# Kernel tuning notes

Measured on AMD Instinct MI355X. Metric: run time of the kernel, lower is better.

## Reference

```python
import jax, jax.numpy as jnp
import numpy as np

NEG_SLOPE = 0.2  # PyG GATConv leaky_relu slope


def _embed(feats, W1, b1, W2, b2, Wc, bc):
    # collapse_esm (two plain Linears, no activation) then linear_comb
    esm = feats[..., 24:] @ W1 + b1
    esm = esm @ W2 + b2
    x = jnp.concatenate([feats[..., :24], esm], axis=-1)
    return x @ Wc + bc


def _gat_conv(x, src, dst, n, W, a_src, a_dst, b, concat):
    # PyG GATConv: project, per-edge attention logits, softmax over incoming edges at dst,
    # weighted scatter-sum. Self loops already included in (src, dst).
    H, C = a_src.shape
    h = (x @ W).reshape(-1, H, C)                 # [N,H,C]
    s = (h * a_src).sum(-1)                       # [N,H]
    d = (h * a_dst).sum(-1)                       # [N,H]
    e = jax.nn.leaky_relu(s[src] + d[dst], NEG_SLOPE)  # [E,H]
    m = jax.ops.segment_max(e, dst, num_segments=n)
    e = jnp.exp(e - m[dst])
    z = jax.ops.segment_sum(e, dst, num_segments=n)
    alpha = e / z[dst]                            # [E,H]
    out = jax.ops.segment_sum(h[src] * alpha[:, :, None], dst, num_segments=n)  # [N,H,C]
    out = out.reshape(n, H * C) if concat else out.mean(axis=1)
    return out + b


def setup_inputs() -> dict:
    key = jax.random.key(0)
    ks = jax.random.split(key, 24)
    N, E, B, F = 100000, 3200000, 8, 50
    NF, M1, M2, M3, CH = 1304, 652, 326, 350, 32
    L, H, HID = 3, 8, 4
    f32 = jnp.float32
    inp = {
        "node_features": jax.random.normal(ks[0], (N, NF), f32),
        "edge_index": jax.random.randint(ks[1], (2, E), 0, N, dtype=jnp.int32),
        "edge_attr": jax.random.normal(ks[2], (E, 8), f32),
        "frag_emb": jax.random.normal(ks[3], (B, F, NF), f32),
        "W_esm1": jax.random.normal(ks[4], (NF - 24, M1), f32) / np.sqrt(NF - 24),
        "b_esm1": jnp.zeros((M1,), f32),
        "W_esm2": jax.random.normal(ks[5], (M1, M2), f32) / np.sqrt(M1),
        "b_esm2": jnp.zeros((M2,), f32),
        "W_comb": jax.random.normal(ks[6], (M3, CH), f32) / np.sqrt(M3),
        "b_comb": jnp.zeros((CH,), f32),
        "gat1_W": jax.random.normal(ks[7], (L, CH, H * HID), f32) / np.sqrt(CH),
        "gat1_asrc": jax.random.normal(ks[8], (L, H, HID), f32) * 0.1,
        "gat1_adst": jax.random.normal(ks[9], (L, H, HID), f32) * 0.1,
        "gat1_b": jnp.zeros((L, H * HID), f32),
        "gat2_W": jax.random.normal(ks[10], (L, H * HID, CH), f32) / np.sqrt(H * HID),
        "gat2_asrc": jax.random.normal(ks[11], (L, 1, CH), f32) * 0.1,
        "gat2_adst": jax.random.normal(ks[12], (L, 1, CH), f32) * 0.1,
        "gat2_b": jnp.zeros((L, CH), f32),
        "W_fin": jax.random.normal(ks[13], (CH, 1), f32) / np.sqrt(CH),
        "b_fin": jnp.zeros((1,), f32),
    }
    return inp


def reference(node_features, edge_index, edge_attr, frag_emb,
              W_esm1, b_esm1, W_esm2, b_esm2, W_comb, b_comb,
              gat1_W, gat1_asrc, gat1_adst, gat1_b,
              gat2_W, gat2_asrc, gat2_adst, gat2_b,
              W_fin, b_fin):
    N = node_features.shape[0]
    loop = jnp.arange(N, dtype=edge_index.dtype)
    src = jnp.concatenate([edge_index[0], loop])  # self loops (PyG default)
    dst = jnp.concatenate([edge_index[1], loop])

    x = _embed(node_features, W_esm1, b_esm1, W_esm2, b_esm2, W_comb, b_comb)  # [N,32]
    for i in range(gat1_W.shape[0]):
        x = _gat_conv(x, src, dst, N, gat1_W[i], gat1_asrc[i], gat1_adst[i], gat1_b[i], True)
        x = jax.nn.elu(x)
        x = _gat_conv(x, src, dst, N, gat2_W[i], gat2_asrc[i], gat2_adst[i], gat2_b[i], False)

    ys = _embed(frag_emb, W_esm1, b_esm1, W_esm2, b_esm2, W_comb, b_comb)  # [B,F,32]
    B, F, C = ys.shape
    xb = x.reshape(B, N // B, C)                      # equal-size graphs
    A = jax.nn.softmax(jnp.einsum('bnd,bfd->bnf', xb, ys), axis=-1)
    p = jnp.einsum('bnf,bfd->bnd', A, ys)             # [B,n,32]
    return jax.nn.sigmoid(p @ W_fin + b_fin).squeeze(-1)  # [B,n]
```

## Files before the change

### kernel.cpp

```cpp
#include <hip/hip_runtime.h>
#include <hip/hip_bf16.h>

#define NF 1304
#define M1 652
#define M2 326
#define CH 32
#define NHEAD1 8
#define HID1 4
#define NLAYER 3
#define FRAG 50
#define NBATCH 8
#define DPAD 32

static inline int ceil_div(int a, int b){ return (a + b - 1)/b; }

__device__ __forceinline__ unsigned short f2h(float f){
  _Float16 h = (_Float16)f;
  unsigned short u;
  __builtin_memcpy(&u, &h, 2);
  return u;
}
__device__ __forceinline__ float h2f(unsigned short u){
  _Float16 h;
  __builtin_memcpy(&h, &u, 2);
  return (float)h;
}

#define TM 64
#define TN 64
#define TKK 16
__global__ __launch_bounds__(256) void gemm_bias(
    const float* __restrict__ A, int lda,
    const float* __restrict__ B, int ldb,
    const float* __restrict__ bias,
    float* __restrict__ C, int ldc,
    int M, int N, int K, int acc)
{
  __shared__ float As[TKK][TM + 1];
  __shared__ float Bs[TKK][TN];
  int tid = threadIdx.x;
  int tx = tid & 15, ty = tid >> 4;
  int row0 = blockIdx.y * TM, col0 = blockIdx.x * TN;
  float c[4][4] = {};
  for (int k0 = 0; k0 < K; k0 += TKK) {
    #pragma unroll
    for (int p = 0; p < 4; ++p) {
      int r = (tid >> 4) + p * 16;
      int kk = tid & 15;
      int gr = row0 + r, gk = k0 + kk;
      float v = 0.f;
      if (gr < M && gk < K) v = A[(long long)gr * lda + gk];
      As[kk][r] = v;
    }
    #pragma unroll
    for (int p = 0; p < 4; ++p) {
      int kk = (tid >> 6) + p * 4;
      int cc = tid & 63;
      int gk = k0 + kk, gc = col0 + cc;
      float v = 0.f;
      if (gk < K && gc < N) v = B[(long long)gk * ldb + gc];
      Bs[kk][cc] = v;
    }
    __syncthreads();
    #pragma unroll
    for (int kk = 0; kk < TKK; ++kk) {
      float a[4], b[4];
      #pragma unroll
      for (int i = 0; i < 4; ++i) a[i] = As[kk][ty + 16 * i];
      #pragma unroll
      for (int j = 0; j < 4; ++j) b[j] = Bs[kk][tx + 16 * j];
      #pragma unroll
      for (int i = 0; i < 4; ++i)
        #pragma unroll
        for (int j = 0; j < 4; ++j)
          c[i][j] += a[i] * b[j];
    }
    __syncthreads();
  }
  #pragma unroll
  for (int i = 0; i < 4; ++i) {
    int gr = row0 + ty + 16 * i;
    if (gr >= M) continue;
    #pragma unroll
    for (int j = 0; j < 4; ++j) {
      int gc = col0 + tx + 16 * j;
      if (gc >= N) continue;
      float v = c[i][j];
      if (bias) v += bias[gc];
      if (acc) v += C[(long long)gr * ldc + gc];
      C[(long long)gr * ldc + gc] = v;
    }
  }
}

__global__ void fold_misc_kernel(const float* __restrict__ Wc, const float* __restrict__ T1,
                                 const float* __restrict__ b1, const float* __restrict__ b2,
                                 const float* __restrict__ bc,
                                 float* __restrict__ Wbig, float* __restrict__ bfold)
{
  int tid = threadIdx.x;
  for (int i = tid; i < 24 * CH; i += 256) Wbig[i] = Wc[i];
  if (tid < CH) {
    float v = bc[tid];
    for (int k = 0; k < M2; ++k) v += b2[k] * Wc[(24 + k) * CH + tid];
    for (int i = 0; i < M1; ++i) v += b1[i] * T1[i * CH + tid];
    bfold[tid] = v;
  }
}

#define EK 64
__global__ __launch_bounds__(256) void gemm_n32(
    const float* __restrict__ A, int M, int K,
    const float* __restrict__ W, const float* __restrict__ bias,
    float* __restrict__ C)
{
  __shared__ float As[64][65];
  __shared__ float Ws[EK][32];
  int tid = threadIdx.x;
  int row0 = blockIdx.x * 64;
  int tx = tid & 7, ty = tid >> 3;
  float c0[4] = {}, c1[4] = {};
  for (int k0 = 0; k0 < K; k0 += EK) {
    #pragma unroll
    for (int p = 0; p < 4; ++p) {
      int q = tid + p * 256;
      int r = q >> 4, c4 = (q & 15) * 4;
      int gr = row0 + r, gk = k0 + c4;
      float4 v = make_float4(0.f, 0.f, 0.f, 0.f);
      if (gr < M) {
        if (gk + 3 < K) v = *(const float4*)&A[(long long)gr * K + gk];
        else {
          float t[4] = {0.f, 0.f, 0.f, 0.f};
          for (int i = 0; i < 4; ++i) if (gk + i < K) t[i] = A[(long long)gr * K + gk + i];
          v = make_float4(t[0], t[1], t[2], t[3]);
        }
      }
      As[r][c4 + 0] = v.x; As[r][c4 + 1] = v.y; As[r][c4 + 2] = v.z; As[r][c4 + 3] = v.w;
    }
    #pragma unroll
    for (int p = 0; p < 2; ++p) {
      int q = tid + p * 256;
      int r = q >> 3, c4 = (q & 7) * 4;
      int gk = k0 + r;
      float4 v = make_float4(0.f, 0.f, 0.f, 0.f);
      if (gk < K) v = *(const float4*)&W[(long long)gk * 32 + c4];
      *(float4*)&Ws[r][c4] = v;
    }
    __syncthreads();
    #pragma unroll
    for (int kk = 0; kk < EK; ++kk) {
      float4 b = *(const float4*)&Ws[kk][tx * 4];
      float a0 = As[ty * 2][kk], a1 = As[ty * 2 + 1][kk];
      c0[0] += a0 * b.x; c0[1] += a0 * b.y; c0[2] += a0 * b.z; c0[3] += a0 * b.w;
      c1[0] += a1 * b.x; c1[1] += a1 * b.y; c1[2] += a1 * b.z; c1[3] += a1 * b.w;
    }
    __syncthreads();
  }
  float4 bb = *(const float4*)&bias[tx * 4];
  int gr0 = row0 + ty * 2;
  if (gr0 < M) {
    float4 v = make_float4(c0[0] + bb.x, c0[1] + bb.y, c0[2] + bb.z, c0[3] + bb.w);
    *(float4*)&C[(long long)gr0 * 32 + tx * 4] = v;
  }
  if (gr0 + 1 < M) {
    float4 v = make_float4(c1[0] + bb.x, c1[1] + bb.y, c1[2] + bb.z, c1[3] + bb.w);
    *(float4*)&C[(long long)(gr0 + 1) * 32 + tx * 4] = v;
  }
}

__global__ void zero_deg_kernel(int* __restrict__ degp, long long n)
{
  long long i = (long long)blockIdx.x * 256 + threadIdx.x;
  if (i < n) degp[i] = 0;
}
__global__ void rank_kernel(const int* __restrict__ ei, int E,
                            int* __restrict__ degp, int* __restrict__ rank)
{
  int e = blockIdx.x * 256 + threadIdx.x;
  if (e < E) rank[e] = atomicAdd(&degp[(long long)ei[E + e] * DPAD], 1);
}
__global__ void partial_kernel(const int* __restrict__ degp, int N, int* __restrict__ partial)
{
  __shared__ int sd[256];
  int i = blockIdx.x * 256 + threadIdx.x;
  sd[threadIdx.x] = (i < N) ? degp[(long long)i * DPAD] : 0;
  __syncthreads();
  for (int off = 128; off > 0; off >>= 1) {
    if (threadIdx.x < off) sd[threadIdx.x] += sd[threadIdx.x + off];
    __syncthreads();
  }
  if (threadIdx.x == 0) partial[blockIdx.x] = sd[0];
}
__global__ void scanp_kernel(int* __restrict__ partial, int NB)
{
  __shared__ int sd[512];
  int t = threadIdx.x;
  int v = (t < NB) ? partial[t] : 0;
  sd[t] = v;
  __syncthreads();
  for (int off = 1; off < 512; off <<= 1) {
    int u = (t >= off) ? sd[t - off] : 0;
    __syncthreads();
    sd[t] += u;
    __syncthreads();
  }
  if (t < NB) partial[t] = sd[t] - v;
}
__global__ void scan_final_kernel(const int* __restrict__ degp, int N,
                                  const int* __restrict__ partial,
                                  int* __restrict__ rowptr)
{
  __shared__ int sd[256];
  int i = blockIdx.x * 256 + threadIdx.x;
  int t = threadIdx.x;
  int v = (i < N) ? degp[(long long)i * DPAD] : 0;
  sd[t] = v;
  __syncthreads();
  for (int off = 1; off < 256; off <<= 1) {
    int u = (t >= off) ? sd[t - off] : 0;
    __syncthreads();
    sd[t] += u;
    __syncthreads();
  }
  if (i < N) {
    int excl = partial[blockIdx.x] + sd[t] - v;
    rowptr[i] = excl;
    if (i == N - 1) rowptr[N] = excl + v;
  }
}
__global__ void scatter_plain_kernel(const int* __restrict__ ei, int E,
                                     const int* __restrict__ rowptr,
                                     const int* __restrict__ rank,
                                     int* __restrict__ csr)
{
  int e = blockIdx.x * 256 + threadIdx.x;
  if (e >= E) return;
  int dn = ei[E + e];
  csr[rowptr[dn] + rank[e]] = ei[e];
}

template<int H, int C>
__global__ __launch_bounds__(256) void proj_sd_kernel(
    const float* __restrict__ x, const float* __restrict__ W,
    const float* __restrict__ asrc, const float* __restrict__ adst,
    unsigned* __restrict__ hp, float* __restrict__ sv, float* __restrict__ dv, int N)
{
  __shared__ float Ws[CH][CH];
  __shared__ float al[2][CH];
  int tid = threadIdx.x;
  for (int i = tid; i < CH * CH; i += 256) Ws[i >> 5][i & 31] = W[i];
  if (tid < CH) { al[0][tid] = asrc[tid]; al[1][tid] = adst[tid]; }
  __syncthreads();
  int n = blockIdx.x * 256 + tid;
  if (n >= N) return;
  float xr[CH];
  #pragma unroll
  for (int j = 0; j < CH / 4; ++j) {
    float4 v = *(const float4*)&x[(long long)n * CH + j * 4];
    xr[j * 4] = v.x; xr[j * 4 + 1] = v.y; xr[j * 4 + 2] = v.z; xr[j * 4 + 3] = v.w;
  }
  float hr[CH] = {};
  #pragma unroll
  for (int c = 0; c < CH; ++c) {
    float xc = xr[c];
    #pragma unroll
    for (int j4 = 0; j4 < CH / 4; ++j4) {
      float4 w = *(const float4*)&Ws[c][j4 * 4];
      hr[j4 * 4] += xc * w.x; hr[j4 * 4 + 1] += xc * w.y;
      hr[j4 * 4 + 2] += xc * w.z; hr[j4 * 4 + 3] += xc * w.w;
    }
  }
  unsigned pk[16];
  #pragma unroll
  for (int j = 0; j < 16; ++j)
    pk[j] = (unsigned)f2h(hr[2 * j]) | ((unsigned)f2h(hr[2 * j + 1]) << 16);
  uint4* hq = (uint4*)&hp[(long long)n * 16];
  #pragma unroll
  for (int j = 0; j < 4; ++j)
    hq[j] = make_uint4(pk[4 * j], pk[4 * j + 1], pk[4 * j + 2], pk[4 * j + 3]);
  #pragma unroll
  for (int hh = 0; hh < H; ++hh) {
    float ss = 0.f, dd = 0.f;
    #pragma unroll
    for (int c = 0; c < C; ++c) {
      float v = hr[hh * C + c];
      ss += v * al[0][hh * C + c];
      dd += v * al[1][hh * C + c];
    }
    sv[(long long)n * H + hh] = ss;
    dv[(long long)n * H + hh] = dd;
  }
}

template<int H, int C>
__global__ __launch_bounds__(256) void gat_gather_kernel(
    const int* __restrict__ rowptr, const int* __restrict__ csr,
    const unsigned* __restrict__ hp, const float* __restrict__ sv,
    const float* __restrict__ dv, const float* __restrict__ bias,
    float* __restrict__ xout, int N, int do_elu)
{
  int wid = threadIdx.x >> 6;
  int lane = threadIdx.x & 63;
  int n = blockIdx.x * 4 + wid;
  if (n >= N) return;
  int cpair = lane & 15;
  int slot = lane >> 4;
  int hh = (C == HID1) ? (cpair >> 1) : 0;
  float dn = dv[(long long)n * H + hh];
  float acc0 = 0.f, acc1 = 0.f, z = 0.f;
  if (slot == 0) {
    float lg = sv[(long long)n * H + hh] + dn;
    lg = lg > 0.f ? lg : 0.2f * lg;
    float w = expf(lg);
    z = w;
    unsigned u = hp[(long long)n * 16 + cpair];
    acc0 = w * h2f((unsigned short)(u & 0xffff));
    acc1 = w * h2f((unsigned short)(u >> 16));
  }
  int start = rowptr[n], end = rowptr[n + 1];
  for (int base = start; base < end; base += 64) {
    int m = end - base; if (m > 64) m = 64;
    int idx = (base + lane < end) ? csr[base + lane] : 0;
    int k = slot;
    for (; k + 12 < m; k += 16) {
      int si0 = __shfl(idx, k, 64);
      int si1 = __shfl(idx, k + 4, 64);
      int si2 = __shfl(idx, k + 8, 64);
      int si3 = __shfl(idx, k + 12, 64);
      float s0 = sv[(long long)si0 * H + hh];
      float s1 = sv[(long long)si1 * H + hh];
      float s2 = sv[(long long)si2 * H + hh];
      float s3 = sv[(long long)si3 * H + hh];
      unsigned u0 = hp[(long long)si0 * 16 + cpair];
      unsigned u1 = hp[(long long)si1 * 16 + cpair];
      unsigned u2 = hp[(long long)si2 * 16 + cpair];
      unsigned u3 = hp[(long long)si3 * 16 + cpair];
      float lg0 = s0 + dn; lg0 = lg0 > 0.f ? lg0 : 0.2f * lg0;
      float lg1 = s1 + dn; lg1 = lg1 > 0.f ? lg1 : 0.2f * lg1;
      float lg2 = s2 + dn; lg2 = lg2 > 0.f ? lg2 : 0.2f * lg2;
      float lg3 = s3 + dn; lg3 = lg3 > 0.f ? lg3 : 0.2f * lg3;
      float w0 = expf(lg0), w1 = expf(lg1), w2 = expf(lg2), w3 = expf(lg3);
      z += (w0 + w1) + (w2 + w3);
      acc0 += w0 * h2f((unsigned short)(u0 & 0xffff))
            + w1 * h2f((unsigned short)(u1 & 0xffff))
            + w2 * h2f((unsigned short)(u2 & 0xffff))
            + w3 * h2f((unsigned short)(u3 & 0xffff));
      acc1 += w0 * h2f((unsigned short)(u0 >> 16))
            + w1 * h2f((unsigned short)(u1 >> 16))
            + w2 * h2f((unsigned short)(u2 >> 16))
            + w3 * h2f((unsigned short)(u3 >> 16));
    }
    for (; k < m; k += 4) {
      int si0 = __shfl(idx, k, 64);
      float s0 = sv[(long long)si0 * H + hh];
      unsigned u0 = hp[(long long)si0 * 16 + cpair];
      float lg0 = s0 + dn; lg0 = lg0 > 0.f ? lg0 : 0.2f * lg0;
      float w0 = expf(lg0);
      z += w0;
      acc0 += w0 * h2f((unsigned short)(u0 & 0xffff));
      acc1 += w0 * h2f((unsigned short)(u0 >> 16));
    }
  }
  acc0 += __shfl_xor(acc0, 16, 64); acc0 += __shfl_xor(acc0, 32, 64);
  acc1 += __shfl_xor(acc1, 16, 64); acc1 += __shfl_xor(acc1, 32, 64);
  z    += __shfl_xor(z, 16, 64);    z    += __shfl_xor(z, 32, 64);
  if (slot == 0) {
    int ch = cpair * 2;
    float v0 = acc0 / z + bias[ch];
    float v1 = acc1 / z + bias[ch + 1];
    if (do_elu) {
      v0 = v0 > 0.f ? v0 : (expf(v0) - 1.f);
      v1 = v1 > 0.f ? v1 : (expf(v1) - 1.f);
    }
    *(float2*)&xout[(long long)n * 32 + ch] = make_float2(v0, v1);
  }
}

__global__ __launch_bounds__(256) void pool_kernel(
    const float* __restrict__ x, const float* __restrict__ ys,
    const float* __restrict__ Wfin, const float* __restrict__ bfin,
    float* __restrict__ out, int NB)
{
  __shared__ float ysl[FRAG][CH];
  __shared__ float tl[FRAG];
  int b = blockIdx.y;
  int tid = threadIdx.x;
  for (int idx = tid; idx < FRAG * CH; idx += 256)
    ysl[idx >> 5][idx & 31] = ys[(long long)b * FRAG * CH + idx];
  __syncthreads();
  if (tid < FRAG) {
    float t = 0.f;
    #pragma unroll
    for (int dd = 0; dd < CH; ++dd) t += ysl[tid][dd] * Wfin[dd];
    tl[tid] = t;
  }
  __syncthreads();
  int n = blockIdx.x * 256 + tid;
  if (n >= NB) return;
  const float* xr = x + ((long long)b * NB + n) * CH;
  float xreg[CH];
  #pragma unroll
  for (int dd = 0; dd < CH; ++dd) xreg[dd] = xr[dd];
  float mx = -1e30f;
  for (int f = 0; f < FRAG; ++f) {
    float l = 0.f;
    #pragma unroll
    for (int dd = 0; dd < CH; ++dd) l += xreg[dd] * ysl[f][dd];
    mx = fmaxf(mx, l);
  }
  float se = 0.f, sw = 0.f;
  for (int f = 0; f < FRAG; ++f) {
    float l = 0.f;
    #pragma unroll
    for (int dd = 0; dd < CH; ++dd) l += xreg[dd] * ysl[f][dd];
    float e = expf(l - mx);
    se += e; sw += e * tl[f];
  }
  float logit = sw / se + bfin[0];
  out[(long long)b * NB + n] = 1.f / (1.f + expf(-logit));
}

extern "C" void kernel_launch(void* const* d_in, const int* in_sizes, int n_in,
                              void* d_out, int out_size, void* d_ws, size_t ws_size,
                              hipStream_t stream)
{
  const float* feats = (const float*)d_in[0];
  const int*   ei    = (const int*)d_in[1];
  const float* frag  = (const float*)d_in[3];
  const float* W1    = (const float*)d_in[4];
  const float* b1    = (const float*)d_in[5];
  const float* W2    = (const float*)d_in[6];
  const float* b2    = (const float*)d_in[7];
  const float* Wc    = (const float*)d_in[8];
  const float* bc    = (const float*)d_in[9];
  const float* g1W   = (const float*)d_in[10];
  const float* g1as  = (const float*)d_in[11];
  const float* g1ad  = (const float*)d_in[12];
  const float* g1b   = (const float*)d_in[13];
  const float* g2W   = (const float*)d_in[14];
  const float* g2as  = (const float*)d_in[15];
  const float* g2ad  = (const float*)d_in[16];
  const float* g2b   = (const float*)d_in[17];
  const float* Wfin  = (const float*)d_in[18];
  const float* bfin  = (const float*)d_in[19];

  const int N  = in_sizes[0] / NF;
  const int E  = in_sizes[1] / 2;
  const int BF = in_sizes[3] / NF;
  const int NB = N / NBATCH;

  char* ws = (char*)d_ws;
  size_t off = 0;
  auto walloc = [&](size_t bytes) -> void* {
    void* p = ws + off;
    off += (bytes + 255) & ~(size_t)255;
    return p;
  };
  float*    T1     = (float*)walloc((size_t)M1 * CH * 4);
  float*    Wbig   = (float*)walloc((size_t)NF * CH * 4);
  float*    bfold  = (float*)walloc((size_t)CH * 4);
  float*    x0     = (float*)walloc((size_t)N * CH * 4);
  float*    x1     = (float*)walloc((size_t)N * CH * 4);
  unsigned* hbuf   = (unsigned*)walloc((size_t)N * 16 * 4);
  float*    sbuf   = (float*)walloc((size_t)N * NHEAD1 * 4);
  float*    dbuf   = (float*)walloc((size_t)N * NHEAD1 * 4);
  float*    ysb    = (float*)walloc((size_t)BF * CH * 4);
  int*      degp   = (int*)walloc((size_t)N * DPAD * 4);
  int*      rowptr = (int*)walloc((size_t)(N + 1) * 4);
  int*      rank   = (int*)walloc((size_t)E * 4);
  int*      part   = (int*)walloc((size_t)512 * 4);
  int*      csr    = (int*)walloc((size_t)E * 4);
  (void)ws_size; (void)n_in; (void)out_size;

  {
    dim3 g1(1, ceil_div(M1, TM));
    gemm_bias<<<g1, 256, 0, stream>>>(W2, M2, Wc + 24 * CH, CH, nullptr, T1, CH,
                                      M1, CH, M2, 0);
    dim3 g2(1, ceil_div(NF - 24, TM));
    gemm_bias<<<g2, 256, 0, stream>>>(W1, M1, T1, CH, nullptr, Wbig + 24 * CH, CH,
                                      NF - 24, CH, M1, 0);
    fold_misc_kernel<<<1, 256, 0, stream>>>(Wc, T1, b1, b2, bc, Wbig, bfold);
  }

  {
    long long npad = (long long)N * DPAD;
    int nb = ceil_div(N, 256);
    zero_deg_kernel<<<(int)((npad + 255) / 256), 256, 0, stream>>>(degp, npad);
    rank_kernel<<<ceil_div(E, 256), 256, 0, stream>>>(ei, E, degp, rank);
    partial_kernel<<<nb, 256, 0, stream>>>(degp, N, part);
    scanp_kernel<<<1, 512, 0, stream>>>(part, nb);
    scan_final_kernel<<<nb, 256, 0, stream>>>(degp, N, part, rowptr);
    scatter_plain_kernel<<<ceil_div(E, 256), 256, 0, stream>>>(ei, E, rowptr, rank, csr);
  }

  gemm_n32<<<ceil_div(N, 64), 256, 0, stream>>>(feats, N, NF, Wbig, bfold, x0);
  gemm_n32<<<ceil_div(BF, 64), 256, 0, stream>>>(frag, BF, NF, Wbig, bfold, ysb);

  auto conv = [&](const float* xin, float* xout, const float* W, const float* as_,
                  const float* ad_, const float* bias, int H, int do_elu) {
    if (H == NHEAD1) {
      proj_sd_kernel<NHEAD1, HID1><<<ceil_div(N, 256), 256, 0, stream>>>(
          xin, W, as_, ad_, hbuf, sbuf, dbuf, N);
      gat_gather_kernel<NHEAD1, HID1><<<ceil_div(N, 4), 256, 0, stream>>>(
          rowptr, csr, hbuf, sbuf, dbuf, bias, xout, N, do_elu);
    } else {
      proj_sd_kernel<1, CH><<<ceil_div(N, 256), 256, 0, stream>>>(
          xin, W, as_, ad_, hbuf, sbuf, dbuf, N);
      gat_gather_kernel<1, CH><<<ceil_div(N, 4), 256, 0, stream>>>(
          rowptr, csr, hbuf, sbuf, dbuf, bias, xout, N, do_elu);
    }
  };

  for (int l = 0; l < NLAYER; ++l) {
    conv(x0, x1, g1W + l * CH * CH, g1as + l * NHEAD1 * HID1, g1ad + l * NHEAD1 * HID1,
         g1b + l * CH, NHEAD1, 1);
    conv(x1, x0, g2W + l * CH * CH, g2as + l * CH, g2ad + l * CH,
         g2b + l * CH, 1, 0);
  }

  pool_kernel<<<dim3(ceil_div(NB, 256), NBATCH), 256, 0, stream>>>(
      x0, ysb, Wfin, bfin, (float*)d_out, NB);
}
```

Measured before the change: 1.346 ms.

## Fuse embed GEMM with edge ranking and recompute source logits in gather

Merges the node-embedding GEMM and the atomic degree/rank pass into one launch, interleaving one GEMM block per eight rank blocks so the compute-bound and atomic-bound work share the GPU. It also drops the per-node source attention logit buffer: the gather kernel recomputes each neighbour's source score from the already-gathered fp16 features via lane shuffles. This removes one scattered load per edge and one store stream, at the cost of extra shuffle reductions per edge, which are longer for the single-head layers.

```diff
diff --git a/kernel.cpp b/kernel.cpp
--- a/kernel.cpp
+++ b/kernel.cpp
@@ -109,15 +109,14 @@
 }
 
 #define EK 64
-__global__ __launch_bounds__(256) void gemm_n32(
+__device__ __forceinline__ void gemm_n32_body(
     const float* __restrict__ A, int M, int K,
     const float* __restrict__ W, const float* __restrict__ bias,
-    float* __restrict__ C)
-{
-  __shared__ float As[64][65];
-  __shared__ float Ws[EK][32];
+    float* __restrict__ C, int bid,
+    float (*As)[65], float (*Ws)[32])
+{
   int tid = threadIdx.x;
-  int row0 = blockIdx.x * 64;
+  int row0 = bid * 64;
   int tx = tid & 7, ty = tid >> 3;
   float c0[4] = {}, c1[4] = {};
   for (int k0 = 0; k0 < K; k0 += EK) {
@@ -168,16 +167,41 @@
   }
 }
 
+__global__ __launch_bounds__(256) void gemm_n32(
+    const float* __restrict__ A, int M, int K,
+    const float* __restrict__ W, const float* __restrict__ bias,
+    float* __restrict__ C)
+{
+  __shared__ float As[64][65];
+  __shared__ float Ws[EK][32];
+  gemm_n32_body(A, M, K, W, bias, C, blockIdx.x, As, Ws);
+}
+
+__global__ __launch_bounds__(256) void fused_embed_rank(
+    const float* __restrict__ A, int M, int K,
+    const float* __restrict__ W, const float* __restrict__ bias,
+    float* __restrict__ C, int nEmbed,
+    const int* __restrict__ ei, int E,
+    int* __restrict__ degp, int* __restrict__ rank)
+{
+  __shared__ float As[64][65];
+  __shared__ float Ws[EK][32];
+  int id = blockIdx.x;
+  if (id % 9 == 0) {
+    int eid = id / 9;
+    if (eid >= nEmbed) return;
+    gemm_n32_body(A, M, K, W, bias, C, eid, As, Ws);
+  } else {
+    int rid = id - id / 9 - 1;
+    long long e = (long long)rid * 256 + threadIdx.x;
+    if (e < E) rank[e] = atomicAdd(&degp[(long long)ei[E + e] * DPAD], 1);
+  }
+}
+
 __global__ void zero_deg_kernel(int* __restrict__ degp, long long n)
 {
   long long i = (long long)blockIdx.x * 256 + threadIdx.x;
   if (i < n) degp[i] = 0;
-}
-__global__ void rank_kernel(const int* __restrict__ ei, int E,
-                            int* __restrict__ degp, int* __restrict__ rank)
-{
-  int e = blockIdx.x * 256 + threadIdx.x;
-  if (e < E) rank[e] = atomicAdd(&degp[(long long)ei[E + e] * DPAD], 1);
 }
 __global__ void partial_kernel(const int* __restrict__ degp, int N, int* __restrict__ partial)
 {
@@ -242,14 +266,14 @@
 template<int H, int C>
 __global__ __launch_bounds__(256) void proj_sd_kernel(
     const float* __restrict__ x, const float* __restrict__ W,
-    const float* __restrict__ asrc, const float* __restrict__ adst,
-    unsigned* __restrict__ hp, float* __restrict__ sv, float* __restrict__ dv, int N)
+    const float* __restrict__ adst,
+    unsigned* __restrict__ hp, float* __restrict__ dv, int N)
 {
   __shared__ float Ws[CH][CH];
-  __shared__ float al[2][CH];
+  __shared__ float al[CH];
   int tid = threadIdx.x;
   for (int i = tid; i < CH * CH; i += 256) Ws[i >> 5][i & 31] = W[i];
-  if (tid < CH) { al[0][tid] = asrc[tid]; al[1][tid] = adst[tid]; }
+  if (tid < CH) al[tid] = adst[tid];
   __syncthreads();
   int n = blockIdx.x * 256 + tid;
   if (n >= N) return;
@@ -280,14 +304,9 @@
     hq[j] = make_uint4(pk[4 * j], pk[4 * j + 1], pk[4 * j + 2], pk[4 * j + 3]);
   #pragma unroll
   for (int hh = 0; hh < H; ++hh) {
-    float ss = 0.f, dd = 0.f;
-    #pragma unroll
-    for (int c = 0; c < C; ++c) {
-      float v = hr[hh * C + c];
-      ss += v * al[0][hh * C + c];
-      dd += v * al[1][hh * C + c];
-    }
-    sv[(long long)n * H + hh] = ss;
+    float dd = 0.f;
+    #pragma unroll
+    for (int c = 0; c < C; ++c) dd += hr[hh * C + c] * al[hh * C + c];
     dv[(long long)n * H + hh] = dd;
   }
 }
@@ -295,7 +314,7 @@
 template<int H, int C>
 __global__ __launch_bounds__(256) void gat_gather_kernel(
     const int* __restrict__ rowptr, const int* __restrict__ csr,
-    const unsigned* __restrict__ hp, const float* __restrict__ sv,
+    const unsigned* __restrict__ hp, const float* __restrict__ asrc,
     const float* __restrict__ dv, const float* __restrict__ bias,
     float* __restrict__ xout, int N, int do_elu)
 {
@@ -305,17 +324,33 @@
   if (n >= N) return;
   int cpair = lane & 15;
   int slot = lane >> 4;
+  int ch = cpair * 2;
   int hh = (C == HID1) ? (cpair >> 1) : 0;
+  float a0 = asrc[ch], a1 = asrc[ch + 1];
   float dn = dv[(long long)n * H + hh];
+
+  auto sred = [&](float p) {
+    p += __shfl_xor(p, 1, 64);
+    if (C == CH) {
+      p += __shfl_xor(p, 2, 64);
+      p += __shfl_xor(p, 4, 64);
+      p += __shfl_xor(p, 8, 64);
+    }
+    return p;
+  };
+
   float acc0 = 0.f, acc1 = 0.f, z = 0.f;
-  if (slot == 0) {
-    float lg = sv[(long long)n * H + hh] + dn;
-    lg = lg > 0.f ? lg : 0.2f * lg;
-    float w = expf(lg);
-    z = w;
+  {
     unsigned u = hp[(long long)n * 16 + cpair];
-    acc0 = w * h2f((unsigned short)(u & 0xffff));
-    acc1 = w * h2f((unsigned short)(u >> 16));
+    float h0 = h2f((unsigned short)(u & 0xffff));
+    float h1 = h2f((unsigned short)(u >> 16));
+    float s = sred(h0 * a0 + h1 * a1);
+    if (slot == 0) {
+      float lg = s + dn;
+      lg = lg > 0.f ? lg : 0.2f * lg;
+      float w = expf(lg);
+      z = w; acc0 = w * h0; acc1 = w * h1;
+    }
   }
   int start = rowptr[n], end = rowptr[n + 1];
   for (int base = start; base < end; base += 64) {
@@ -327,45 +362,43 @@
       int si1 = __shfl(idx, k + 4, 64);
       int si2 = __shfl(idx, k + 8, 64);
       int si3 = __shfl(idx, k + 12, 64);
-      float s0 = sv[(long long)si0 * H + hh];
-      float s1 = sv[(long long)si1 * H + hh];
-      float s2 = sv[(long long)si2 * H + hh];
-      float s3 = sv[(long long)si3 * H + hh];
       unsigned u0 = hp[(long long)si0 * 16 + cpair];
       unsigned u1 = hp[(long long)si1 * 16 + cpair];
       unsigned u2 = hp[(long long)si2 * 16 + cpair];
       unsigned u3 = hp[(long long)si3 * 16 + cpair];
+      float h00 = h2f((unsigned short)(u0 & 0xffff)), h01 = h2f((unsigned short)(u0 >> 16));
+      float h10 = h2f((unsigned short)(u1 & 0xffff)), h11 = h2f((unsigned short)(u1 >> 16));
+      float h20 = h2f((unsigned short)(u2 & 0xffff)), h21 = h2f((unsigned short)(u2 >> 16));
+      float h30 = h2f((unsigned short)(u3 & 0xffff)), h31 = h2f((unsigned short)(u3 >> 16));
+      float s0 = sred(h00 * a0 + h01 * a1);
+      float s1 = sred(h10 * a0 + h11 * a1);
+      float s2 = sred(h20 * a0 + h21 * a1);
+      float s3 = sred(h30 * a0 + h31 * a1);
       float lg0 = s0 + dn; lg0 = lg0 > 0.f ? lg0 : 0.2f * lg0;
       float lg1 = s1 + dn; lg1 = lg1 > 0.f ? lg1 : 0.2f * lg1;
       float lg2 = s2 + dn; lg2 = lg2 > 0.f ? lg2 : 0.2f * lg2;
       float lg3 = s3 + dn; lg3 = lg3 > 0.f ? lg3 : 0.2f * lg3;
       float w0 = expf(lg0), w1 = expf(lg1), w2 = expf(lg2), w3 = expf(lg3);
       z += (w0 + w1) + (w2 + w3);
-      acc0 += w0 * h2f((unsigned short)(u0 & 0xffff))
-            + w1 * h2f((unsigned short)(u1 & 0xffff))
-            + w2 * h2f((unsigned short)(u2 & 0xffff))
-            + w3 * h2f((unsigned short)(u3 & 0xffff));
-      acc1 += w0 * h2f((unsigned short)(u0 >> 16))
-            + w1 * h2f((unsigned short)(u1 >> 16))
-            + w2 * h2f((unsigned short)(u2 >> 16))
-            + w3 * h2f((unsigned short)(u3 >> 16));
+      acc0 += w0 * h00 + w1 * h10 + w2 * h20 + w3 * h30;
+      acc1 += w0 * h01 + w1 * h11 + w2 * h21 + w3 * h31;
     }
     for (; k < m; k += 4) {
       int si0 = __shfl(idx, k, 64);
-      float s0 = sv[(long long)si0 * H + hh];
       unsigned u0 = hp[(long long)si0 * 16 + cpair];
+      float h00 = h2f((unsigned short)(u0 & 0xffff)), h01 = h2f((unsigned short)(u0 >> 16));
+      float s0 = sred(h00 * a0 + h01 * a1);
       float lg0 = s0 + dn; lg0 = lg0 > 0.f ? lg0 : 0.2f * lg0;
       float w0 = expf(lg0);
       z += w0;
-      acc0 += w0 * h2f((unsigned short)(u0 & 0xffff));
-      acc1 += w0 * h2f((unsigned short)(u0 >> 16));
+      acc0 += w0 * h00;
+      acc1 += w0 * h01;
     }
   }
   acc0 += __shfl_xor(acc0, 16, 64); acc0 += __shfl_xor(acc0, 32, 64);
   acc1 += __shfl_xor(acc1, 16, 64); acc1 += __shfl_xor(acc1, 32, 64);
   z    += __shfl_xor(z, 16, 64);    z    += __shfl_xor(z, 32, 64);
   if (slot == 0) {
-    int ch = cpair * 2;
     float v0 = acc0 / z + bias[ch];
     float v1 = acc1 / z + bias[ch + 1];
     if (do_elu) {
@@ -462,7 +495,6 @@
   float*    x0     = (float*)walloc((size_t)N * CH * 4);
   float*    x1     = (float*)walloc((size_t)N * CH * 4);
   unsigned* hbuf   = (unsigned*)walloc((size_t)N * 16 * 4);
-  float*    sbuf   = (float*)walloc((size_t)N * NHEAD1 * 4);
   float*    dbuf   = (float*)walloc((size_t)N * NHEAD1 * 4);
   float*    ysb    = (float*)walloc((size_t)BF * CH * 4);
   int*      degp   = (int*)walloc((size_t)N * DPAD * 4);
@@ -484,30 +516,39 @@
 
   {
     long long npad = (long long)N * DPAD;
+    zero_deg_kernel<<<(int)((npad + 255) / 256), 256, 0, stream>>>(degp, npad);
+    int nEmbed = ceil_div(N, 64);
+    int rankB = ceil_div(E, 256);
+    int G = 9 * nEmbed;
+    int embedSlots = (G + 8) / 9;
+    int rankSlots = G - embedSlots;
+    if (rankSlots < rankB) G += (rankB - rankSlots) * 9 / 8 + 9;
+    fused_embed_rank<<<G, 256, 0, stream>>>(feats, N, NF, Wbig, bfold, x0,
+                                            nEmbed, ei, E, degp, rank);
+  }
+
+  {
     int nb = ceil_div(N, 256);
-    zero_deg_kernel<<<(int)((npad + 255) / 256), 256, 0, stream>>>(degp, npad);
-    rank_kernel<<<ceil_div(E, 256), 256, 0, stream>>>(ei, E, degp, rank);
     partial_kernel<<<nb, 256, 0, stream>>>(degp, N, part);
     scanp_kernel<<<1, 512, 0, stream>>>(part, nb);
     scan_final_kernel<<<nb, 256, 0, stream>>>(degp, N, part, rowptr);
     scatter_plain_kernel<<<ceil_div(E, 256), 256, 0, stream>>>(ei, E, rowptr, rank, csr);
   }
 
-  gemm_n32<<<ceil_div(N, 64), 256, 0, stream>>>(feats, N, NF, Wbig, bfold, x0);
   gemm_n32<<<ceil_div(BF, 64), 256, 0, stream>>>(frag, BF, NF, Wbig, bfold, ysb);
 
   auto conv = [&](const float* xin, float* xout, const float* W, const float* as_,
                   const float* ad_, const float* bias, int H, int do_elu) {
     if (H == NHEAD1) {
       proj_sd_kernel<NHEAD1, HID1><<<ceil_div(N, 256), 256, 0, stream>>>(
-          xin, W, as_, ad_, hbuf, sbuf, dbuf, N);
+          xin, W, ad_, hbuf, dbuf, N);
       gat_gather_kernel<NHEAD1, HID1><<<ceil_div(N, 4), 256, 0, stream>>>(
-          rowptr, csr, hbuf, sbuf, dbuf, bias, xout, N, do_elu);
+          rowptr, csr, hbuf, as_, dbuf, bias, xout, N, do_elu);
     } else {
       proj_sd_kernel<1, CH><<<ceil_div(N, 256), 256, 0, stream>>>(
-          xin, W, as_, ad_, hbuf, sbuf, dbuf, N);
+          xin, W, ad_, hbuf, dbuf, N);
       gat_gather_kernel<1, CH><<<ceil_div(N, 4), 256, 0, stream>>>(
-          rowptr, csr, hbuf, sbuf, dbuf, bias, xout, N, do_elu);
+          rowptr, csr, hbuf, as_, dbuf, bias, xout, N, do_elu);
     }
   };
 
```

Result: no change. 1.331 ms (-1.1%).
